# Optimization experiments

Measured on AMD Instinct MI355X. Metric: run time of the kernel, lower is better.

## Reference

```python
import jax, jax.numpy as jnp
import numpy as np

B, M, N, E, H, HID = 4, 512, 512, 256, 16, 16
D = E // H


def setup_inputs() -> dict:
    key = jax.random.key(0)
    ks = jax.random.split(key, 10)
    u = lambda k, shape, lim: jax.random.uniform(k, shape, jnp.float32, -lim, lim)
    mix1_init = (1.0 / 2.0) ** 0.5
    mix2_init = (1.0 / 16.0) ** 0.5
    return {
        "q_input": jax.random.normal(ks[0], (B, M, E), jnp.float32),
        "kv_input": jax.random.normal(ks[1], (B, N, E), jnp.float32),
        "dmat": jax.random.uniform(ks[2], (B, M, N), jnp.float32),
        "Wq": u(ks[3], (E, E), 1.0 / np.sqrt(E)),
        "Wkv": u(ks[4], (2 * E, E), 1.0 / np.sqrt(E)),
        "mix_W1": u(ks[5], (H, 2, HID), mix1_init),
        "mix_b1": u(ks[6], (H, HID), mix1_init),
        "mix_W2": u(ks[7], (H, HID, 1), mix2_init),
        "mix_b2": u(ks[8], (H, 1), mix2_init),
        "Wout": u(ks[9], (E, E), 1.0 / np.sqrt(E)),
    }


def reference(q_input, kv_input, dmat, Wq, Wkv, mix_W1, mix_b1, mix_W2, mix_b2, Wout):
    b, m, e = q_input.shape
    n = kv_input.shape[1]
    h = mix_W1.shape[0]
    d = e // h
    # projections (torch Linear: y = x @ W.T)
    q = (q_input @ Wq.T).reshape(b, m, h, d).transpose(0, 2, 1, 3)        # b h m d
    kv = (kv_input @ Wkv.T).reshape(b, n, 2, h, d)                        # (two h d) split
    k = kv[:, :, 0].transpose(0, 2, 1, 3)                                 # b h n d
    v = kv[:, :, 1].transpose(0, 2, 1, 3)                                 # b h n d
    scale = jnp.sqrt(jnp.asarray(d, q.dtype))
    scores = jnp.einsum('bhmd,bhnd->bhmn', q, k) / scale                  # b h m n
    # mix scores with dmat via per-head 2-layer MLP on the last (size-2) axis
    mix = jnp.stack([scores, jnp.broadcast_to(dmat[:, None], scores.shape)], axis=-1)  # b h m n 2
    hidden = jax.nn.relu(jnp.einsum('bhmnt,htk->bhmnk', mix, mix_W1)
                         + mix_b1[None, :, None, None, :])                # b h m n HID
    mixed = (jnp.einsum('bhmnk,hko->bhmno', hidden, mix_W2)
             + mix_b2[None, :, None, None, :])[..., 0]                    # b h m n
    probs = jax.nn.softmax(mixed, axis=-1)
    out = jnp.einsum('bhmn,bhnd->bhmd', probs, v)                         # b h m d
    out = out.transpose(0, 2, 1, 3).reshape(b, m, e)                      # b m (h d)
    return out @ Wout.T
```

## Files before the change

kernel.cpp:

```cpp
#include <hip/hip_runtime.h>
#include <stdint.h>
#include <stddef.h>

#define MM 512
#define NN 512
#define EE 256
#define HH 16
#define DD 16

typedef __bf16 bf16x8 __attribute__((ext_vector_type(8)));
typedef float f32x4 __attribute__((ext_vector_type(4)));

static __device__ __forceinline__ bf16x8 bzero8() {
  bf16x8 z;
#pragma unroll
  for (int i = 0; i < 8; ++i) z[i] = (__bf16)0.0f;
  return z;
}

static __device__ __forceinline__ bf16x8 cvt8(const float* __restrict__ p) {
  const float4 u = *(const float4*)p;
  const float4 v = *(const float4*)(p + 4);
  bf16x8 r;
  r[0] = (__bf16)u.x; r[1] = (__bf16)u.y; r[2] = (__bf16)u.z; r[3] = (__bf16)u.w;
  r[4] = (__bf16)v.x; r[5] = (__bf16)v.y; r[6] = (__bf16)v.z; r[7] = (__bf16)v.w;
  return r;
}

static __device__ __forceinline__ unsigned short f2b(float f) {
  union { __bf16 h; unsigned short u; } cv;
  cv.h = (__bf16)f;
  return cv.u;
}

static __device__ __forceinline__ float b2f(unsigned short u) {
  union { unsigned int i; float f; } cv;
  cv.i = ((unsigned int)u) << 16;
  return cv.f;
}

static __device__ __forceinline__ float fexp2(float x) {
  float r;
  asm("v_exp_f32 %0, %1" : "=v"(r) : "v"(x));
  return r;
}

static __device__ __forceinline__ unsigned int cvtpk(float lo, float hi) {
  unsigned int r;
  asm("v_cvt_pk_bf16_f32 %0, %1, %2" : "=v"(r) : "v"(lo), "v"(hi));
  return r;
}

static __device__ __forceinline__ float sload(const float* p) {
  return __int_as_float(__builtin_amdgcn_readfirstlane(__float_as_int(*p)));
}

__global__ __launch_bounds__(256) void proj_all_kernel(
    const float* __restrict__ Xq, const float* __restrict__ Xkv,
    const float* __restrict__ Wq, const float* __restrict__ Wkv,
    const float* __restrict__ Wout,
    unsigned short* __restrict__ Qs, unsigned short* __restrict__ Ks,
    unsigned short* __restrict__ Vt,
    unsigned short* __restrict__ Whi, unsigned short* __restrict__ Wlo) {
  const int by = blockIdx.y;
  const int tid = threadIdx.x;

  if (by == 12) {
    const int base = (blockIdx.x * 256 + tid) * 4;
    const float4 v = *(const float4*)(Wout + base);
    float c4[4] = {v.x, v.y, v.z, v.w};
#pragma unroll
    for (int i = 0; i < 4; ++i) {
      const unsigned short hb = f2b(c4[i]);
      Whi[base + i] = hb;
      Wlo[base + i] = f2b(c4[i] - b2f(hb));
    }
    return;
  }

  const int w = tid >> 6, l = tid & 63;
  const int lg = l >> 4, lr = l & 15;
  const int t0 = blockIdx.x * 32 + (w & 1) * 16;

  if (by < 4) {
    const int n0 = by * 64 + (w >> 1) * 32;
    f32x4 acc0 = {0.f, 0.f, 0.f, 0.f}, acc1 = {0.f, 0.f, 0.f, 0.f};
#pragma unroll
    for (int kc = 0; kc < EE; kc += 32) {
      const int k = kc + lg * 8;
      bf16x8 a  = cvt8(Xq + (size_t)(t0 + lr) * EE + k);
      bf16x8 b0 = cvt8(Wq + (size_t)(n0 + lr) * EE + k);
      bf16x8 b1 = cvt8(Wq + (size_t)(n0 + 16 + lr) * EE + k);
      acc0 = __builtin_amdgcn_mfma_f32_16x16x32_bf16(a, b0, acc0, 0, 0, 0);
      acc1 = __builtin_amdgcn_mfma_f32_16x16x32_bf16(a, b1, acc1, 0, 0, 0);
    }
#pragma unroll
    for (int r = 0; r < 4; ++r) {
      const int t = t0 + 4 * lg + r, b = t >> 9, m = t & 511;
      const int j0 = n0 + lr, j1 = j0 + 16;
      Qs[((size_t)(b * HH + (j0 >> 4)) * MM + m) * DD + (j0 & 15)] = f2b(acc0[r] * 0.25f);
      Qs[((size_t)(b * HH + (j1 >> 4)) * MM + m) * DD + (j1 & 15)] = f2b(acc1[r] * 0.25f);
    }
  } else {
    const int n0 = (by - 4) * 64 + (w >> 1) * 32;
    f32x4 acc0 = {0.f, 0.f, 0.f, 0.f}, acc1 = {0.f, 0.f, 0.f, 0.f};
#pragma unroll
    for (int kc = 0; kc < EE; kc += 32) {
      const int k = kc + lg * 8;
      bf16x8 a  = cvt8(Xkv + (size_t)(t0 + lr) * EE + k);
      bf16x8 b0 = cvt8(Wkv + (size_t)(n0 + lr) * EE + k);
      bf16x8 b1 = cvt8(Wkv + (size_t)(n0 + 16 + lr) * EE + k);
      acc0 = __builtin_amdgcn_mfma_f32_16x16x32_bf16(a, b0, acc0, 0, 0, 0);
      acc1 = __builtin_amdgcn_mfma_f32_16x16x32_bf16(a, b1, acc1, 0, 0, 0);
    }
#pragma unroll
    for (int r = 0; r < 4; ++r) {
      const int t = t0 + 4 * lg + r, b = t >> 9, n = t & 511;
#pragma unroll
      for (int fi = 0; fi < 2; ++fi) {
        const int j = n0 + lr + fi * 16;
        const float v = fi ? acc1[r] : acc0[r];
        if (j < 256) {
          Ks[((size_t)(b * HH + (j >> 4)) * NN + n) * DD + (j & 15)] = f2b(v);
        } else {
          const int jj = j - 256;
          Vt[((size_t)(b * HH + (jj >> 4)) * DD + (jj & 15)) * NN + n] = f2b(v);
        }
      }
    }
  }
}

__global__ __launch_bounds__(256, 4) void attn_kernel(
    const unsigned short* __restrict__ Qs, const unsigned short* __restrict__ Ks,
    const unsigned short* __restrict__ Vt, const float* __restrict__ dmat,
    const float* __restrict__ W1, const float* __restrict__ b1v,
    const float* __restrict__ W2,
    unsigned short* __restrict__ Ahi, unsigned short* __restrict__ Alo) {
  __shared__ unsigned short P[32][520];
  __shared__ float red[4][32];
  float (*pvred)[2][16][16] = (float (*)[2][16][16]) & P[0][0];

  const int tid = threadIdx.x, w = tid >> 6, l = tid & 63;
  const int lg = l >> 4, lr = l & 15;
  const int bid = blockIdx.x;
  const int mt = bid & 15, hh = (bid >> 4) & 15, b = bid >> 8;
  const int m0 = mt * 32;
  const int n0 = w * 128;

  const unsigned short* Qbase = Qs + ((size_t)(b * HH + hh) * MM + m0) * DD;
  const unsigned short* Kbase = Ks + (size_t)(b * HH + hh) * NN * DD;
  const unsigned short* Vbase = Vt + (size_t)(b * HH + hh) * DD * NN;
  const float* dbase = dmat + (size_t)b * MM * NN;

  float ckv[16], bkv[16], wkp[16];
  float Ac = 0.f, Cc = 0.f;
  const float hiln2 = 0.5f * 1.4426950408889634f;
#pragma unroll
  for (int k = 0; k < 16; ++k) {
    const float ak = sload(W1 + hh * 32 + k);
    const float ck = sload(W1 + hh * 32 + 16 + k);
    const float bk = sload(b1v + hh * 16 + k);
    const float wk = hiln2 * sload(W2 + hh * 16 + k);
    Ac += wk * ak;
    Cc += wk * ck;
    const float ra = 1.0f / ak;
    ckv[k] = ck * ra;
    bkv[k] = bk * ra;
    wkp[k] = wk * fabsf(ak);
    asm volatile("" : "+v"(ckv[k]));
    asm volatile("" : "+v"(bkv[k]));
  }

  bf16x8 qb[2];
#pragma unroll
  for (int mb = 0; mb < 2; ++mb) {
    qb[mb] = bzero8();
    if (lg < 2) qb[mb] = *(const bf16x8*)(Qbase + (mb * 16 + lr) * DD + lg * 8);
  }

  const f32x4 zf = {0.f, 0.f, 0.f, 0.f};
  float psum[2] = {0.f, 0.f};

  const float* dpl0 = dbase + (size_t)(m0 + lr) * NN + n0 + 4 * lg;
  const float* dpl1 = dbase + (size_t)(m0 + 16 + lr) * NN + n0 + 4 * lg;

  float4 dva0 = *(const float4*)(dpl0);
  float4 dva1 = *(const float4*)(dpl1);
  bf16x8 ka0 = bzero8();
  if (lg < 2) ka0 = *(const bf16x8*)(Kbase + (size_t)(n0 + lr) * DD + lg * 8);

#pragma unroll
  for (int nb = 0; nb < 8; ++nb) {
    float4 dvb0, dvb1;
    bf16x8 ka1 = bzero8();
    if (nb < 7) {
      dvb0 = *(const float4*)(dpl0 + (nb + 1) * 16);
      dvb1 = *(const float4*)(dpl1 + (nb + 1) * 16);
      if (lg < 2)
        ka1 = *(const bf16x8*)(Kbase + (size_t)(n0 + (nb + 1) * 16 + lr) * DD + lg * 8);
    }

    f32x4 cc[2];
    cc[0] = __builtin_amdgcn_mfma_f32_16x16x32_bf16(ka0, qb[0], zf, 0, 0, 0);
    cc[1] = __builtin_amdgcn_mfma_f32_16x16x32_bf16(ka0, qb[1], zf, 0, 0, 0);

#pragma unroll
    for (int mb = 0; mb < 2; ++mb) {
      const float4 dvv = mb ? dva1 : dva0;
      float ev[4];
#pragma unroll
      for (int r = 0; r < 4; ++r) {
        const float s = cc[mb][r];
        const float d = (r == 0) ? dvv.x : (r == 1) ? dvv.y : (r == 2) ? dvv.z : dvv.w;
        float acc = fmaf(Ac, s, Cc * d);
#pragma unroll
        for (int k = 0; k < 16; ++k) {
          const float t = fmaf(ckv[k], d, bkv[k]);
          acc = fmaf(wkp[k], fabsf(s + t), acc);
        }
        const float e = fexp2(acc);
        psum[mb] += e;
        ev[r] = e;
      }
      uint2 u;
      u.x = cvtpk(ev[0], ev[1]);
      u.y = cvtpk(ev[2], ev[3]);
      *(uint2*)&P[mb * 16 + lr][n0 + nb * 16 + 4 * lg] = u;
    }

    dva0 = dvb0;
    dva1 = dvb1;
    ka0 = ka1;
  }

#pragma unroll
  for (int mb = 0; mb < 2; ++mb) {
    psum[mb] += __shfl_xor(psum[mb], 16);
    psum[mb] += __shfl_xor(psum[mb], 32);
    if (lg == 0) red[w][mb * 16 + lr] = psum[mb];
  }

  f32x4 pv[2];
  pv[0] = zf; pv[1] = zf;
#pragma unroll
  for (int kb = 0; kb < 4; ++kb) {
    const bf16x8 vb = *(const bf16x8*)(Vbase + (size_t)lr * NN + (n0 + kb * 32 + lg * 8));
#pragma unroll
    for (int mb = 0; mb < 2; ++mb) {
      const bf16x8 pa = *(const bf16x8*)(&P[mb * 16 + lr][n0 + kb * 32 + lg * 8]);
      pv[mb] = __builtin_amdgcn_mfma_f32_16x16x32_bf16(pa, vb, pv[mb], 0, 0, 0);
    }
  }
  __syncthreads();
#pragma unroll
  for (int mb = 0; mb < 2; ++mb)
#pragma unroll
    for (int r = 0; r < 4; ++r) pvred[w][mb][4 * lg + r][lr] = pv[mb][r];
  __syncthreads();

  for (int i = tid; i < 512; i += 256) {
    const int mr = i >> 4, dd = i & 15;
    const float s = pvred[0][mr >> 4][mr & 15][dd] + pvred[1][mr >> 4][mr & 15][dd] +
                    pvred[2][mr >> 4][mr & 15][dd] + pvred[3][mr >> 4][mr & 15][dd];
    const float rs = red[0][mr] + red[1][mr] + red[2][mr] + red[3][mr];
    const float val = s / rs;
    const unsigned short hb = f2b(val);
    const size_t o = ((size_t)(b * MM) + m0 + mr) * EE + hh * DD + dd;
    Ahi[o] = hb;
    Alo[o] = f2b(val - b2f(hb));
  }
}

__global__ __launch_bounds__(256) void out_gemm_kernel(
    const unsigned short* __restrict__ Ahi, const unsigned short* __restrict__ Alo,
    const unsigned short* __restrict__ Whi, const unsigned short* __restrict__ Wlo,
    float* __restrict__ out) {
  const int tid = threadIdx.x, w = tid >> 6, l = tid & 63;
  const int lg = l >> 4, lr = l & 15;
  const int t0 = blockIdx.x * 32 + (w & 1) * 16;
  const int n0 = blockIdx.y * 64 + (w >> 1) * 32;
  f32x4 acc0 = {0.f, 0.f, 0.f, 0.f}, acc1 = {0.f, 0.f, 0.f, 0.f};
#pragma unroll
  for (int kc = 0; kc < EE; kc += 32) {
    const int k = kc + lg * 8;
    const bf16x8 ah = *(const bf16x8*)(Ahi + (size_t)(t0 + lr) * EE + k);
    const bf16x8 al = *(const bf16x8*)(Alo + (size_t)(t0 + lr) * EE + k);
    const bf16x8 bh0 = *(const bf16x8*)(Whi + (size_t)(n0 + lr) * EE + k);
    const bf16x8 bh1 = *(const bf16x8*)(Whi + (size_t)(n0 + 16 + lr) * EE + k);
    const bf16x8 bl0 = *(const bf16x8*)(Wlo + (size_t)(n0 + lr) * EE + k);
    const bf16x8 bl1 = *(const bf16x8*)(Wlo + (size_t)(n0 + 16 + lr) * EE + k);
    acc0 = __builtin_amdgcn_mfma_f32_16x16x32_bf16(ah, bh0, acc0, 0, 0, 0);
    acc0 = __builtin_amdgcn_mfma_f32_16x16x32_bf16(al, bh0, acc0, 0, 0, 0);
    acc0 = __builtin_amdgcn_mfma_f32_16x16x32_bf16(ah, bl0, acc0, 0, 0, 0);
    acc1 = __builtin_amdgcn_mfma_f32_16x16x32_bf16(ah, bh1, acc1, 0, 0, 0);
    acc1 = __builtin_amdgcn_mfma_f32_16x16x32_bf16(al, bh1, acc1, 0, 0, 0);
    acc1 = __builtin_amdgcn_mfma_f32_16x16x32_bf16(ah, bl1, acc1, 0, 0, 0);
  }
#pragma unroll
  for (int r = 0; r < 4; ++r) {
    const int row = t0 + 4 * lg + r;
    out[(size_t)row * EE + n0 + lr] = acc0[r];
    out[(size_t)row * EE + n0 + 16 + lr] = acc1[r];
  }
}

extern "C" void kernel_launch(void* const* d_in, const int* in_sizes, int n_in,
                              void* d_out, int out_size, void* d_ws, size_t ws_size,
                              hipStream_t stream) {
  const float* q_input  = (const float*)d_in[0];
  const float* kv_input = (const float*)d_in[1];
  const float* dmat     = (const float*)d_in[2];
  const float* Wq       = (const float*)d_in[3];
  const float* Wkv      = (const float*)d_in[4];
  const float* W1       = (const float*)d_in[5];
  const float* b1       = (const float*)d_in[6];
  const float* W2       = (const float*)d_in[7];
  const float* Wout     = (const float*)d_in[9];
  float* out = (float*)d_out;

  char* ws = (char*)d_ws;
  unsigned short* Qs  = (unsigned short*)(ws);
  unsigned short* Ks  = (unsigned short*)(ws + (1u << 20));
  unsigned short* Vt  = (unsigned short*)(ws + (2u << 20));
  unsigned short* Ahi = (unsigned short*)(ws + (3u << 20));
  unsigned short* Alo = (unsigned short*)(ws + (4u << 20));
  unsigned short* Whi = (unsigned short*)(ws + (5u << 20));
  unsigned short* Wlo = (unsigned short*)(ws + (5u << 20) + (1u << 17));

  proj_all_kernel<<<dim3(64, 13), 256, 0, stream>>>(q_input, kv_input, Wq, Wkv, Wout,
                                                    Qs, Ks, Vt, Whi, Wlo);
  attn_kernel<<<dim3(1024), 256, 0, stream>>>(Qs, Ks, Vt, dmat, W1, b1, W2,
                                              Ahi, Alo);
  out_gemm_kernel<<<dim3(64, 4), 256, 0, stream>>>(Ahi, Alo, Whi, Wlo, out);
}
```

Before: 63.64 us.

## Fuse output projection into attention kernel via last-block atomic counter

Removes the separate output GEMM launch. Each attention block bumps a per-(batch, row-tile) atomic counter, and the last of the 16 head blocks for that row tile computes the 32x256 output projection from Ahi/Alo. The block index mapping is also remapped so that blocks sharing a row tile land on the same XCD, which should help L2 locality for the Ahi/Alo reads. This saves one kernel launch and its tail, but the output GEMM now runs serialized inside only 64 last blocks, and the fence and atomic add overhead to every block.

```diff
diff --git a/kernel.cpp b/kernel.cpp
--- a/kernel.cpp
+++ b/kernel.cpp
@@ -61,11 +61,13 @@
     const float* __restrict__ Wout,
     unsigned short* __restrict__ Qs, unsigned short* __restrict__ Ks,
     unsigned short* __restrict__ Vt,
-    unsigned short* __restrict__ Whi, unsigned short* __restrict__ Wlo) {
+    unsigned short* __restrict__ Whi, unsigned short* __restrict__ Wlo,
+    unsigned int* __restrict__ cnt) {
   const int by = blockIdx.y;
   const int tid = threadIdx.x;
 
   if (by == 12) {
+    if (blockIdx.x == 0 && tid < 64) cnt[tid] = 0u;
     const int base = (blockIdx.x * 256 + tid) * 4;
     const float4 v = *(const float4*)(Wout + base);
     float c4[4] = {v.x, v.y, v.z, v.w};
@@ -136,15 +138,21 @@
     const unsigned short* __restrict__ Vt, const float* __restrict__ dmat,
     const float* __restrict__ W1, const float* __restrict__ b1v,
     const float* __restrict__ W2,
-    unsigned short* __restrict__ Ahi, unsigned short* __restrict__ Alo) {
+    unsigned short* __restrict__ Ahi, unsigned short* __restrict__ Alo,
+    const unsigned short* __restrict__ Whi, const unsigned short* __restrict__ Wlo,
+    float* __restrict__ out, unsigned int* __restrict__ cnt) {
   __shared__ unsigned short P[32][520];
   __shared__ float red[4][32];
+  __shared__ int lastf;
   float (*pvred)[2][16][16] = (float (*)[2][16][16]) & P[0][0];
 
   const int tid = threadIdx.x, w = tid >> 6, l = tid & 63;
   const int lg = l >> 4, lr = l & 15;
   const int bid = blockIdx.x;
-  const int mt = bid & 15, hh = (bid >> 4) & 15, b = bid >> 8;
+  const int xcd = bid & 7, slot = bid >> 3;
+  const int hh = slot & 15;
+  const int g = (slot >> 4) * 8 + xcd;
+  const int b = g >> 4, mt = g & 15;
   const int m0 = mt * 32;
   const int n0 = w * 128;
 
@@ -270,38 +278,38 @@
     Ahi[o] = hb;
     Alo[o] = f2b(val - b2f(hb));
   }
-}
-
-__global__ __launch_bounds__(256) void out_gemm_kernel(
-    const unsigned short* __restrict__ Ahi, const unsigned short* __restrict__ Alo,
-    const unsigned short* __restrict__ Whi, const unsigned short* __restrict__ Wlo,
-    float* __restrict__ out) {
-  const int tid = threadIdx.x, w = tid >> 6, l = tid & 63;
-  const int lg = l >> 4, lr = l & 15;
-  const int t0 = blockIdx.x * 32 + (w & 1) * 16;
-  const int n0 = blockIdx.y * 64 + (w >> 1) * 32;
-  f32x4 acc0 = {0.f, 0.f, 0.f, 0.f}, acc1 = {0.f, 0.f, 0.f, 0.f};
-#pragma unroll
-  for (int kc = 0; kc < EE; kc += 32) {
-    const int k = kc + lg * 8;
-    const bf16x8 ah = *(const bf16x8*)(Ahi + (size_t)(t0 + lr) * EE + k);
-    const bf16x8 al = *(const bf16x8*)(Alo + (size_t)(t0 + lr) * EE + k);
-    const bf16x8 bh0 = *(const bf16x8*)(Whi + (size_t)(n0 + lr) * EE + k);
-    const bf16x8 bh1 = *(const bf16x8*)(Whi + (size_t)(n0 + 16 + lr) * EE + k);
-    const bf16x8 bl0 = *(const bf16x8*)(Wlo + (size_t)(n0 + lr) * EE + k);
-    const bf16x8 bl1 = *(const bf16x8*)(Wlo + (size_t)(n0 + 16 + lr) * EE + k);
-    acc0 = __builtin_amdgcn_mfma_f32_16x16x32_bf16(ah, bh0, acc0, 0, 0, 0);
-    acc0 = __builtin_amdgcn_mfma_f32_16x16x32_bf16(al, bh0, acc0, 0, 0, 0);
-    acc0 = __builtin_amdgcn_mfma_f32_16x16x32_bf16(ah, bl0, acc0, 0, 0, 0);
-    acc1 = __builtin_amdgcn_mfma_f32_16x16x32_bf16(ah, bh1, acc1, 0, 0, 0);
-    acc1 = __builtin_amdgcn_mfma_f32_16x16x32_bf16(al, bh1, acc1, 0, 0, 0);
-    acc1 = __builtin_amdgcn_mfma_f32_16x16x32_bf16(ah, bl1, acc1, 0, 0, 0);
-  }
-#pragma unroll
-  for (int r = 0; r < 4; ++r) {
-    const int row = t0 + 4 * lg + r;
-    out[(size_t)row * EE + n0 + lr] = acc0[r];
-    out[(size_t)row * EE + n0 + 16 + lr] = acc1[r];
+
+  if (tid == 0) {
+    __threadfence();
+    const unsigned int old = __hip_atomic_fetch_add(
+        &cnt[g], 1u, __ATOMIC_ACQ_REL, __HIP_MEMORY_SCOPE_AGENT);
+    lastf = (old == 15u) ? 1 : 0;
+  }
+  __syncthreads();
+  if (lastf) {
+    __threadfence();
+    const int rbase = b * MM + m0 + (w & 1) * 16;
+    const int c0 = (w >> 1) * 128;
+    f32x4 acc[8] = {zf, zf, zf, zf, zf, zf, zf, zf};
+#pragma unroll
+    for (int kc = 0; kc < EE; kc += 32) {
+      const int k = kc + lg * 8;
+      const bf16x8 ah = *(const bf16x8*)(Ahi + (size_t)(rbase + lr) * EE + k);
+      const bf16x8 al = *(const bf16x8*)(Alo + (size_t)(rbase + lr) * EE + k);
+#pragma unroll
+      for (int t = 0; t < 8; ++t) {
+        const bf16x8 bh = *(const bf16x8*)(Whi + (size_t)(c0 + t * 16 + lr) * EE + k);
+        const bf16x8 bl = *(const bf16x8*)(Wlo + (size_t)(c0 + t * 16 + lr) * EE + k);
+        acc[t] = __builtin_amdgcn_mfma_f32_16x16x32_bf16(ah, bh, acc[t], 0, 0, 0);
+        acc[t] = __builtin_amdgcn_mfma_f32_16x16x32_bf16(al, bh, acc[t], 0, 0, 0);
+        acc[t] = __builtin_amdgcn_mfma_f32_16x16x32_bf16(ah, bl, acc[t], 0, 0, 0);
+      }
+    }
+#pragma unroll
+    for (int t = 0; t < 8; ++t)
+#pragma unroll
+      for (int r = 0; r < 4; ++r)
+        out[(size_t)(rbase + 4 * lg + r) * EE + c0 + t * 16 + lr] = acc[t][r];
   }
 }
 
@@ -327,10 +335,10 @@
   unsigned short* Alo = (unsigned short*)(ws + (4u << 20));
   unsigned short* Whi = (unsigned short*)(ws + (5u << 20));
   unsigned short* Wlo = (unsigned short*)(ws + (5u << 20) + (1u << 17));
+  unsigned int*   cnt = (unsigned int*)(ws + (5u << 20) + (2u << 17));
 
   proj_all_kernel<<<dim3(64, 13), 256, 0, stream>>>(q_input, kv_input, Wq, Wkv, Wout,
-                                                    Qs, Ks, Vt, Whi, Wlo);
+                                                    Qs, Ks, Vt, Whi, Wlo, cnt);
   attn_kernel<<<dim3(1024), 256, 0, stream>>>(Qs, Ks, Vt, dmat, W1, b1, W2,
-                                              Ahi, Alo);
-  out_gemm_kernel<<<dim3(64, 4), 256, 0, stream>>>(Ahi, Alo, Whi, Wlo, out);
-}
+                                              Ahi, Alo, Whi, Wlo, out, cnt);
+}
```

Measured after the change: 173.4 us. 2.72x slower.

## Pre-convert dmat to bf16, remap attention blocks per XCD, relax occupancy hint

Applied to the files above, without the earlier changes.

The projection kernel gains a 14th block row that converts dmat to bf16 in workspace, and the attention kernel reads these halved dmat tiles instead of fp32. The attention block index is remapped so that all 16 heads sharing a (batch, m-tile) dmat slab land on the same XCD, which should improve L2 reuse of dmat. The launch_bounds occupancy hint drops from 4 to 2, giving the compiler more registers. The cost is an extra full pass over dmat (read fp32, write bf16) plus lower precision of dmat inside the mixing MLP.

```diff
diff --git a/kernel.cpp b/kernel.cpp
--- a/kernel.cpp
+++ b/kernel.cpp
@@ -39,6 +39,13 @@
   return cv.f;
 }
 
+static __device__ __forceinline__ float b2f_lo(unsigned int u) {
+  return __int_as_float((int)(u << 16));
+}
+static __device__ __forceinline__ float b2f_hi(unsigned int u) {
+  return __int_as_float((int)(u & 0xffff0000u));
+}
+
 static __device__ __forceinline__ float fexp2(float x) {
   float r;
   asm("v_exp_f32 %0, %1" : "=v"(r) : "v"(x));
@@ -58,12 +65,27 @@
 __global__ __launch_bounds__(256) void proj_all_kernel(
     const float* __restrict__ Xq, const float* __restrict__ Xkv,
     const float* __restrict__ Wq, const float* __restrict__ Wkv,
-    const float* __restrict__ Wout,
+    const float* __restrict__ Wout, const float* __restrict__ dmat,
     unsigned short* __restrict__ Qs, unsigned short* __restrict__ Ks,
     unsigned short* __restrict__ Vt,
-    unsigned short* __restrict__ Whi, unsigned short* __restrict__ Wlo) {
+    unsigned short* __restrict__ Whi, unsigned short* __restrict__ Wlo,
+    unsigned short* __restrict__ dmatb) {
   const int by = blockIdx.y;
   const int tid = threadIdx.x;
+
+  if (by == 13) {
+    const int base = blockIdx.x * 256 + tid;
+#pragma unroll
+    for (int it = 0; it < 16; ++it) {
+      const int i4 = it * 16384 + base;
+      const float4 v = *(const float4*)(dmat + (size_t)i4 * 4);
+      uint2 u;
+      u.x = cvtpk(v.x, v.y);
+      u.y = cvtpk(v.z, v.w);
+      *(uint2*)(dmatb + (size_t)i4 * 4) = u;
+    }
+    return;
+  }
 
   if (by == 12) {
     const int base = (blockIdx.x * 256 + tid) * 4;
@@ -131,9 +153,9 @@
   }
 }
 
-__global__ __launch_bounds__(256, 4) void attn_kernel(
+__global__ __launch_bounds__(256, 2) void attn_kernel(
     const unsigned short* __restrict__ Qs, const unsigned short* __restrict__ Ks,
-    const unsigned short* __restrict__ Vt, const float* __restrict__ dmat,
+    const unsigned short* __restrict__ Vt, const unsigned short* __restrict__ dmatb,
     const float* __restrict__ W1, const float* __restrict__ b1v,
     const float* __restrict__ W2,
     unsigned short* __restrict__ Ahi, unsigned short* __restrict__ Alo) {
@@ -144,14 +166,17 @@
   const int tid = threadIdx.x, w = tid >> 6, l = tid & 63;
   const int lg = l >> 4, lr = l & 15;
   const int bid = blockIdx.x;
-  const int mt = bid & 15, hh = (bid >> 4) & 15, b = bid >> 8;
+  const int xcd = bid & 7, slot = bid >> 3;
+  const int hh = slot & 15;
+  const int g = (slot >> 4) * 8 + xcd;
+  const int b = g >> 4, mt = g & 15;
   const int m0 = mt * 32;
   const int n0 = w * 128;
 
   const unsigned short* Qbase = Qs + ((size_t)(b * HH + hh) * MM + m0) * DD;
   const unsigned short* Kbase = Ks + (size_t)(b * HH + hh) * NN * DD;
   const unsigned short* Vbase = Vt + (size_t)(b * HH + hh) * DD * NN;
-  const float* dbase = dmat + (size_t)b * MM * NN;
+  const unsigned short* dbase = dmatb + (size_t)b * MM * NN;
 
   float ckv[16], bkv[16], wkp[16];
   float Ac = 0.f, Cc = 0.f;
@@ -182,21 +207,21 @@
   const f32x4 zf = {0.f, 0.f, 0.f, 0.f};
   float psum[2] = {0.f, 0.f};
 
-  const float* dpl0 = dbase + (size_t)(m0 + lr) * NN + n0 + 4 * lg;
-  const float* dpl1 = dbase + (size_t)(m0 + 16 + lr) * NN + n0 + 4 * lg;
-
-  float4 dva0 = *(const float4*)(dpl0);
-  float4 dva1 = *(const float4*)(dpl1);
+  const unsigned short* dpl0 = dbase + (size_t)(m0 + lr) * NN + n0 + 4 * lg;
+  const unsigned short* dpl1 = dbase + (size_t)(m0 + 16 + lr) * NN + n0 + 4 * lg;
+
+  uint2 dva0 = *(const uint2*)(dpl0);
+  uint2 dva1 = *(const uint2*)(dpl1);
   bf16x8 ka0 = bzero8();
   if (lg < 2) ka0 = *(const bf16x8*)(Kbase + (size_t)(n0 + lr) * DD + lg * 8);
 
 #pragma unroll
   for (int nb = 0; nb < 8; ++nb) {
-    float4 dvb0, dvb1;
+    uint2 dvb0, dvb1;
     bf16x8 ka1 = bzero8();
     if (nb < 7) {
-      dvb0 = *(const float4*)(dpl0 + (nb + 1) * 16);
-      dvb1 = *(const float4*)(dpl1 + (nb + 1) * 16);
+      dvb0 = *(const uint2*)(dpl0 + (nb + 1) * 16);
+      dvb1 = *(const uint2*)(dpl1 + (nb + 1) * 16);
       if (lg < 2)
         ka1 = *(const bf16x8*)(Kbase + (size_t)(n0 + (nb + 1) * 16 + lr) * DD + lg * 8);
     }
@@ -207,12 +232,17 @@
 
 #pragma unroll
     for (int mb = 0; mb < 2; ++mb) {
-      const float4 dvv = mb ? dva1 : dva0;
+      const uint2 dvv = mb ? dva1 : dva0;
+      float dunp[4];
+      dunp[0] = b2f_lo(dvv.x);
+      dunp[1] = b2f_hi(dvv.x);
+      dunp[2] = b2f_lo(dvv.y);
+      dunp[3] = b2f_hi(dvv.y);
       float ev[4];
 #pragma unroll
       for (int r = 0; r < 4; ++r) {
         const float s = cc[mb][r];
-        const float d = (r == 0) ? dvv.x : (r == 1) ? dvv.y : (r == 2) ? dvv.z : dvv.w;
+        const float d = dunp[r];
         float acc = fmaf(Ac, s, Cc * d);
 #pragma unroll
         for (int k = 0; k < 16; ++k) {
@@ -320,17 +350,18 @@
   float* out = (float*)d_out;
 
   char* ws = (char*)d_ws;
-  unsigned short* Qs  = (unsigned short*)(ws);
-  unsigned short* Ks  = (unsigned short*)(ws + (1u << 20));
-  unsigned short* Vt  = (unsigned short*)(ws + (2u << 20));
-  unsigned short* Ahi = (unsigned short*)(ws + (3u << 20));
-  unsigned short* Alo = (unsigned short*)(ws + (4u << 20));
-  unsigned short* Whi = (unsigned short*)(ws + (5u << 20));
-  unsigned short* Wlo = (unsigned short*)(ws + (5u << 20) + (1u << 17));
-
-  proj_all_kernel<<<dim3(64, 13), 256, 0, stream>>>(q_input, kv_input, Wq, Wkv, Wout,
-                                                    Qs, Ks, Vt, Whi, Wlo);
-  attn_kernel<<<dim3(1024), 256, 0, stream>>>(Qs, Ks, Vt, dmat, W1, b1, W2,
+  unsigned short* Qs    = (unsigned short*)(ws);
+  unsigned short* Ks    = (unsigned short*)(ws + (1u << 20));
+  unsigned short* Vt    = (unsigned short*)(ws + (2u << 20));
+  unsigned short* Ahi   = (unsigned short*)(ws + (3u << 20));
+  unsigned short* Alo   = (unsigned short*)(ws + (4u << 20));
+  unsigned short* Whi   = (unsigned short*)(ws + (5u << 20));
+  unsigned short* Wlo   = (unsigned short*)(ws + (5u << 20) + (1u << 17));
+  unsigned short* dmatb = (unsigned short*)(ws + (6u << 20));
+
+  proj_all_kernel<<<dim3(64, 14), 256, 0, stream>>>(q_input, kv_input, Wq, Wkv, Wout,
+                                                    dmat, Qs, Ks, Vt, Whi, Wlo, dmatb);
+  attn_kernel<<<dim3(1024), 256, 0, stream>>>(Qs, Ks, Vt, dmatb, W1, b1, W2,
                                               Ahi, Alo);
   out_gemm_kernel<<<dim3(64, 4), 256, 0, stream>>>(Ahi, Alo, Whi, Wlo, out);
 }
```

Result: faster. 61.81 us, median of 2 (-2.9%).
